# Optimization experiments

Measured on AMD Instinct MI355X. Metric: run time of the kernel, lower is better.

Reference implementation:

```python
import jax, jax.numpy as jnp
import numpy as np

N = 50000      # num_nodes
F_IN = 128     # num_features
E = 800000     # num edges (before self-loops)
H1, D1 = 8, 16 # conv1: 8 heads x 16 dims -> 128 concat
D2 = 8         # conv2: 1 head x 8 dims
NEG_SLOPE = 0.2


def setup_inputs() -> dict:
    key = jax.random.key(0)
    ks = jax.random.split(key, 16)
    s = 0.05
    return {
        "x": jax.random.normal(ks[0], (N, F_IN), jnp.float32),
        "edge_index": jax.random.randint(ks[1], (2, E), 0, N, dtype=jnp.int64),
        "W1": jax.random.normal(ks[2], (F_IN, H1 * D1), jnp.float32) * s,
        "att_src1": jax.random.normal(ks[3], (H1, D1), jnp.float32) * s,
        "att_dst1": jax.random.normal(ks[4], (H1, D1), jnp.float32) * s,
        "b1": jnp.zeros((H1 * D1,), jnp.float32),
        "W2": jax.random.normal(ks[5], (H1 * D1, D2), jnp.float32) * s,
        "att_src2": jax.random.normal(ks[6], (1, D2), jnp.float32) * s,
        "att_dst2": jax.random.normal(ks[7], (1, D2), jnp.float32) * s,
        "b2": jnp.zeros((D2,), jnp.float32),
        "fc1_w": jax.random.normal(ks[8], (N * D2, 84), jnp.float32) * 0.005,
        "fc1_b": jnp.zeros((84,), jnp.float32),
        "fc2_w": jax.random.normal(ks[9], (84, 24), jnp.float32) * s,
        "fc2_b": jnp.zeros((24,), jnp.float32),
        "fc3_w": jax.random.normal(ks[10], (24, 2), jnp.float32) * s,
        "fc3_b": jnp.zeros((2,), jnp.float32),
    }


def gat_conv(x, src, dst, W, att_src, att_dst, bias, heads, out_dim):
    """PyG GATConv: per-head linear, edge attention, scatter-softmax over
    incoming edges per target node, weighted scatter-add aggregation."""
    n = x.shape[0]
    h = (x @ W).reshape(n, heads, out_dim)            # [N,H,D]
    a_src = jnp.einsum('nhd,hd->nh', h, att_src)      # [N,H]
    a_dst = jnp.einsum('nhd,hd->nh', h, att_dst)      # [N,H]
    e = jax.nn.leaky_relu(a_src[src] + a_dst[dst], NEG_SLOPE)  # [Et,H]
    # softmax over edges grouped by destination node (stable)
    m = jax.ops.segment_max(e, dst, num_segments=n)
    p = jnp.exp(e - m[dst])
    denom = jax.ops.segment_sum(p, dst, num_segments=n)
    alpha = p / denom[dst]                            # [Et,H]
    out = jax.ops.segment_sum(alpha[:, :, None] * h[src], dst, num_segments=n)
    return out.reshape(n, heads * out_dim) + bias


def reference(x, edge_index, W1, att_src1, att_dst1, b1,
              W2, att_src2, att_dst2, b2,
              fc1_w, fc1_b, fc2_w, fc2_b, fc3_w, fc3_b):
    # add self-loops (GATConv default add_self_loops=True)
    loop = jnp.arange(N, dtype=edge_index.dtype)
    src = jnp.concatenate([edge_index[0], loop])
    dst = jnp.concatenate([edge_index[1], loop])

    h = jax.nn.elu(gat_conv(x, src, dst, W1, att_src1, att_dst1, b1, H1, D1))
    h = jax.nn.elu(gat_conv(h, src, dst, W2, att_src2, att_dst2, b2, 1, D2))

    z = h.reshape(1, N * D2)                          # batch of one graph
    z = jax.nn.elu(z @ fc1_w + fc1_b)
    z = jax.nn.elu(z @ fc2_w + fc2_b)
    z = z @ fc3_w + fc3_b
    return jax.nn.log_softmax(z, axis=1)              # [1,2]
```

## Files before the change

### kernel.cpp

```cpp
#include <hip/hip_runtime.h>
#include <math.h>

#define N_NODES 50000
#define F_IN 128
#define NE 800000
#define NH1 8
#define ND1 16
#define ND2 8
#define NEG 0.2f
#define ZLEN (N_NODES * ND2)
#define NBLK 196
#define FC1_RPB 240
#define FC1_NB 1667

typedef __attribute__((ext_vector_type(8))) short bf16x8;
typedef __attribute__((ext_vector_type(4))) float f32x4;

__device__ __forceinline__ float lrelu(float v) { return v > 0.f ? v : NEG * v; }
__device__ __forceinline__ float elu1(float v)  { return v > 0.f ? v : (__expf(v) - 1.f); }

__device__ __forceinline__ unsigned short f2bf(float f) {
    union { float f; unsigned int i; } c; c.f = f;
    unsigned int u = c.i;
    return (unsigned short)((u + 0x7FFFu + ((u >> 16) & 1u)) >> 16);
}
__device__ __forceinline__ float bflo(unsigned int u) {
    union { unsigned int i; float f; } c; c.i = u << 16; return c.f;
}
__device__ __forceinline__ float bfhi(unsigned int u) {
    union { unsigned int i; float f; } c; c.i = u & 0xFFFF0000u; return c.f;
}
__device__ __forceinline__ int ei_is64(const int* __restrict__ ei) {
    return ((ei[1] | ei[3] | ei[5] | ei[7]) == 0) ? 1 : 0;
}

__global__ __launch_bounds__(256) void prep_kernel(const float* __restrict__ W,
                                                   uint4* __restrict__ wbf,
                                                   int* __restrict__ counts) {
    int i = blockIdx.x * 256 + threadIdx.x;
    if (i < N_NODES) counts[i] = 1;
    if (i < 2048) {
        int col = i >> 4, kc = i & 15;
        unsigned int u[4];
        #pragma unroll
        for (int jj = 0; jj < 4; ++jj) {
            unsigned int lo = f2bf(W[(kc * 8 + 2 * jj) * 128 + col]);
            unsigned int hi = f2bf(W[(kc * 8 + 2 * jj + 1) * 128 + col]);
            u[jj] = lo | (hi << 16);
        }
        uint4 v; v.x = u[0]; v.y = u[1]; v.z = u[2]; v.w = u[3];
        wbf[col * 16 + (kc ^ (col & 15))] = v;
    }
}

__global__ void hist_kernel(const int* __restrict__ ei, int* __restrict__ counts) {
    int t = blockIdx.x * blockDim.x + threadIdx.x;
    if (t * 4 >= NE) return;
    int d0, d1, d2, d3;
    if (ei_is64(ei)) {
        const int4* p = reinterpret_cast<const int4*>(ei + 2 * NE);
        int4 a = p[t * 2];
        int4 b = p[t * 2 + 1];
        d0 = a.x; d1 = a.z; d2 = b.x; d3 = b.z;
    } else {
        int4 a = reinterpret_cast<const int4*>(ei + NE)[t];
        d0 = a.x; d1 = a.y; d2 = a.z; d3 = a.w;
    }
    atomicAdd(&counts[d0], 1);
    atomicAdd(&counts[d1], 1);
    atomicAdd(&counts[d2], 1);
    atomicAdd(&counts[d3], 1);
}

__global__ __launch_bounds__(256) void scan1_kernel(const int* __restrict__ counts,
                                                    int* __restrict__ bsum) {
    const int t = threadIdx.x;
    int i = blockIdx.x * 256 + t;
    int v = (i < N_NODES) ? counts[i] : 0;
    #pragma unroll
    for (int off = 32; off; off >>= 1) v += __shfl_down(v, off, 64);
    __shared__ int ws[4];
    if ((t & 63) == 0) ws[t >> 6] = v;
    __syncthreads();
    if (t == 0) bsum[blockIdx.x] = ws[0] + ws[1] + ws[2] + ws[3];
}

__global__ __launch_bounds__(256) void scan3_kernel(const int* __restrict__ counts,
                                                    const int* __restrict__ bsum,
                                                    int* __restrict__ rowptr,
                                                    int* __restrict__ cursor) {
    __shared__ int wsum[4];
    __shared__ int wpre[4];
    __shared__ int s_boff;
    const int t = threadIdx.x;
    const int lane = t & 63, w = t >> 6;
    int i = blockIdx.x * 256 + t;
    int v = (i < N_NODES) ? counts[i] : 0;
    int incl = v;
    #pragma unroll
    for (int off = 1; off < 64; off <<= 1) {
        int u = __shfl_up(incl, off, 64);
        if (lane >= off) incl += u;
    }
    if (lane == 63) wsum[w] = incl;
    if (t < 64) {
        int s = 0;
        for (int k = t; k < blockIdx.x; k += 64) s += bsum[k];
        #pragma unroll
        for (int off = 32; off; off >>= 1) s += __shfl_down(s, off, 64);
        if (t == 0) s_boff = s;
    }
    __syncthreads();
    if (t == 0) { int s = 0; for (int j = 0; j < 4; ++j) { wpre[j] = s; s += wsum[j]; } }
    __syncthreads();
    incl += wpre[w] + s_boff;
    if (i < N_NODES) { rowptr[i + 1] = incl; cursor[i] = incl - v; }
    if (i == 0) rowptr[0] = 0;
}

__global__ void fill_kernel(const int* __restrict__ ei,
                            int* __restrict__ cursor, int* __restrict__ esrc) {
    const int t = blockIdx.x * blockDim.x + threadIdx.x;
    const int NT_E = NE / 4;
    if (t < NT_E) {
        int s0, s1, s2, s3, d0, d1, d2, d3;
        if (ei_is64(ei)) {
            const int4* ps = reinterpret_cast<const int4*>(ei);
            const int4* pd = reinterpret_cast<const int4*>(ei + 2 * NE);
            int4 sa = ps[t * 2], sb = ps[t * 2 + 1];
            int4 da = pd[t * 2], db = pd[t * 2 + 1];
            s0 = sa.x; s1 = sa.z; s2 = sb.x; s3 = sb.z;
            d0 = da.x; d1 = da.z; d2 = db.x; d3 = db.z;
        } else {
            int4 sa = reinterpret_cast<const int4*>(ei)[t];
            int4 da = reinterpret_cast<const int4*>(ei + NE)[t];
            s0 = sa.x; s1 = sa.y; s2 = sa.z; s3 = sa.w;
            d0 = da.x; d1 = da.y; d2 = da.z; d3 = da.w;
        }
        esrc[atomicAdd(&cursor[d0], 1)] = s0;
        esrc[atomicAdd(&cursor[d1], 1)] = s1;
        esrc[atomicAdd(&cursor[d2], 1)] = s2;
        esrc[atomicAdd(&cursor[d3], 1)] = s3;
    } else {
        int i = t - NT_E;
        if (i < N_NODES) esrc[atomicAdd(&cursor[i], 1)] = i;
    }
}

__global__ __launch_bounds__(256) void gemm1_kernel(const float* __restrict__ x,
                                                    const uint4* __restrict__ wbf,
                                                    const float* __restrict__ att_src,
                                                    const float* __restrict__ att_dst,
                                                    unsigned int* __restrict__ h1b,
                                                    float* __restrict__ a_src1,
                                                    float* __restrict__ a_dst1) {
    __shared__ uint4 Xs[1024];
    __shared__ uint4 Ws[2048];
    const int t = threadIdx.x;
    const int row0 = blockIdx.x * 64;

    #pragma unroll
    for (int p = 0; p < 8; ++p) Ws[p * 256 + t] = wbf[p * 256 + t];

    #pragma unroll
    for (int p = 0; p < 4; ++p) {
        int cidx = p * 256 + t;
        int row = cidx >> 4, c = cidx & 15;
        int grow = row0 + row;
        float4 xa = make_float4(0.f, 0.f, 0.f, 0.f);
        float4 xb = make_float4(0.f, 0.f, 0.f, 0.f);
        if (grow < N_NODES) {
            xa = *reinterpret_cast<const float4*>(x + (size_t)grow * F_IN + c * 8);
            xb = *reinterpret_cast<const float4*>(x + (size_t)grow * F_IN + c * 8 + 4);
        }
        uint4 u;
        u.x = (unsigned int)f2bf(xa.x) | ((unsigned int)f2bf(xa.y) << 16);
        u.y = (unsigned int)f2bf(xa.z) | ((unsigned int)f2bf(xa.w) << 16);
        u.z = (unsigned int)f2bf(xb.x) | ((unsigned int)f2bf(xb.y) << 16);
        u.w = (unsigned int)f2bf(xb.z) | ((unsigned int)f2bf(xb.w) << 16);
        Xs[row * 16 + (c ^ (row & 15))] = u;
    }
    __syncthreads();

    const int wv = t >> 6;
    const int l  = t & 63;
    const int d  = l & 15;
    const int g  = l >> 4;
    const int arow = wv * 16 + d;

    f32x4 acc[8];
    #pragma unroll
    for (int n = 0; n < 8; ++n) { acc[n][0] = 0.f; acc[n][1] = 0.f; acc[n][2] = 0.f; acc[n][3] = 0.f; }

    #pragma unroll
    for (int ks = 0; ks < 4; ++ks) {
        int kc = ks * 4 + g;
        union { uint4 u; bf16x8 v; } A;
        A.u = Xs[arow * 16 + (kc ^ d)];
        #pragma unroll
        for (int n = 0; n < 8; ++n) {
            union { uint4 u; bf16x8 v; } B;
            B.u = Ws[(n * 16 + d) * 16 + (kc ^ d)];
            acc[n] = __builtin_amdgcn_mfma_f32_16x16x32_bf16(A.v, B.v, acc[n], 0, 0, 0);
        }
    }

    float as8[8], ad8[8];
    #pragma unroll
    for (int n = 0; n < 8; ++n) { as8[n] = att_src[n * 16 + d]; ad8[n] = att_dst[n * 16 + d]; }
    #pragma unroll
    for (int n = 0; n < 8; ++n) {
        #pragma unroll
        for (int r = 0; r < 4; ++r) {
            float ps = acc[n][r] * as8[n];
            float pd = acc[n][r] * ad8[n];
            #pragma unroll
            for (int off = 1; off < 16; off <<= 1) {
                ps += __shfl_xor(ps, off, 16);
                pd += __shfl_xor(pd, off, 16);
            }
            int grow = row0 + wv * 16 + g * 4 + r;
            if (d == 0 && grow < N_NODES) {
                a_src1[grow * 8 + n] = ps;
                a_dst1[grow * 8 + n] = pd;
            }
        }
    }
    #pragma unroll
    for (int n = 0; n < 8; ++n) {
        #pragma unroll
        for (int r = 0; r < 4; ++r) {
            float lo = acc[n][r];
            float hi = __shfl_xor(lo, 1, 64);
            int grow = row0 + wv * 16 + g * 4 + r;
            if (((d & 1) == 0) && grow < N_NODES) {
                unsigned int u = (unsigned int)f2bf(lo) | ((unsigned int)f2bf(hi) << 16);
                h1b[(size_t)grow * 64 + n * 8 + (d >> 1)] = u;
            }
        }
    }
}

__global__ __launch_bounds__(256) void agg1_kernel(const unsigned int* __restrict__ h1b,
                                                   const float* __restrict__ a_src,
                                                   const float* __restrict__ a_dst,
                                                   const int* __restrict__ rowptr,
                                                   const int* __restrict__ esrc,
                                                   const float* __restrict__ b1,
                                                   float* __restrict__ hout) {
    int wid = (blockIdx.x * 256 + threadIdx.x) >> 6;
    if (wid >= N_NODES) return;
    const int lane = threadIdx.x & 63;
    const int h = lane >> 3;
    const float ad = a_dst[wid * 8 + h];
    float acc0 = 0.f, acc1 = 0.f, den = 0.f;
    int j = rowptr[wid];
    const int jend = rowptr[wid + 1];
    for (; j + 8 <= jend; j += 8) {
        int s[8];
        #pragma unroll
        for (int k = 0; k < 8; ++k) s[k] = esrc[j + k];
        unsigned int u[8];
        #pragma unroll
        for (int k = 0; k < 8; ++k) u[k] = h1b[(size_t)s[k] * 64 + lane];
        float e[8];
        #pragma unroll
        for (int k = 0; k < 8; ++k) e[k] = a_src[s[k] * 8 + h];
        #pragma unroll
        for (int k = 0; k < 8; ++k) {
            float p = __expf(lrelu(e[k] + ad));
            den += p;
            acc0 = fmaf(p, bflo(u[k]), acc0);
            acc1 = fmaf(p, bfhi(u[k]), acc1);
        }
    }
    for (; j + 4 <= jend; j += 4) {
        int s0 = esrc[j], s1 = esrc[j + 1], s2 = esrc[j + 2], s3 = esrc[j + 3];
        unsigned int u0 = h1b[(size_t)s0 * 64 + lane];
        unsigned int u1 = h1b[(size_t)s1 * 64 + lane];
        unsigned int u2 = h1b[(size_t)s2 * 64 + lane];
        unsigned int u3 = h1b[(size_t)s3 * 64 + lane];
        float e0 = a_src[s0 * 8 + h], e1 = a_src[s1 * 8 + h];
        float e2 = a_src[s2 * 8 + h], e3 = a_src[s3 * 8 + h];
        float p0 = __expf(lrelu(e0 + ad));
        float p1 = __expf(lrelu(e1 + ad));
        float p2 = __expf(lrelu(e2 + ad));
        float p3 = __expf(lrelu(e3 + ad));
        den += (p0 + p1) + (p2 + p3);
        acc0 = fmaf(p0, bflo(u0), acc0); acc1 = fmaf(p0, bfhi(u0), acc1);
        acc0 = fmaf(p1, bflo(u1), acc0); acc1 = fmaf(p1, bfhi(u1), acc1);
        acc0 = fmaf(p2, bflo(u2), acc0); acc1 = fmaf(p2, bfhi(u2), acc1);
        acc0 = fmaf(p3, bflo(u3), acc0); acc1 = fmaf(p3, bfhi(u3), acc1);
    }
    for (; j < jend; ++j) {
        int s = esrc[j];
        unsigned int u = h1b[(size_t)s * 64 + lane];
        float e = a_src[s * 8 + h];
        float p = __expf(lrelu(e + ad));
        den += p;
        acc0 = fmaf(p, bflo(u), acc0);
        acc1 = fmaf(p, bfhi(u), acc1);
    }
    float inv = 1.f / den;
    float2 bb = *reinterpret_cast<const float2*>(b1 + 2 * lane);
    float o0 = elu1(acc0 * inv + bb.x);
    float o1 = elu1(acc1 * inv + bb.y);
    *reinterpret_cast<float2*>(hout + (size_t)wid * F_IN + 2 * lane) = make_float2(o0, o1);
}

__global__ __launch_bounds__(256) void gemm2_kernel(const float* __restrict__ h,
                                                    const float* __restrict__ W2,
                                                    const float* __restrict__ att_src2,
                                                    const float* __restrict__ att_dst2,
                                                    float* __restrict__ h2,
                                                    float* __restrict__ a_src2,
                                                    float* __restrict__ a_dst2) {
    __shared__ float Ws[F_IN * ND2];
    __shared__ float Hs[32 * 132];
    int t = threadIdx.x;
    int node0 = blockIdx.x * 32;
    #pragma unroll
    for (int i = 0; i < 4; ++i) { int idx = i * 256 + t; Ws[idx] = W2[idx]; }
    #pragma unroll
    for (int i = 0; i < 4; ++i) {
        int fidx = i * 256 + t;
        int r = fidx >> 5;
        int c4 = fidx & 31;
        int grow = node0 + r;
        float4 v = make_float4(0.f, 0.f, 0.f, 0.f);
        if (grow < N_NODES) v = *reinterpret_cast<const float4*>(h + (size_t)grow * F_IN + c4 * 4);
        *reinterpret_cast<float4*>(&Hs[r * 132 + c4 * 4]) = v;
    }
    __syncthreads();
    int nsub = t >> 3, d = t & 7;
    int node = node0 + nsub;
    float acc = 0.f;
    #pragma unroll 8
    for (int k = 0; k < F_IN; ++k)
        acc = fmaf(Hs[nsub * 132 + k], Ws[k * ND2 + d], acc);
    float vs = acc * att_src2[d];
    float vd = acc * att_dst2[d];
    #pragma unroll
    for (int off = 4; off >= 1; off >>= 1) {
        vs += __shfl_xor(vs, off, 8);
        vd += __shfl_xor(vd, off, 8);
    }
    if (node < N_NODES) {
        h2[node * ND2 + d] = acc;
        if (d == 0) { a_src2[node] = vs; a_dst2[node] = vd; }
    }
}

__global__ void agg2_kernel(const float* __restrict__ h2,
                            const float* __restrict__ a_src2, const float* __restrict__ a_dst2,
                            const int* __restrict__ rowptr, const int* __restrict__ esrc,
                            const float* __restrict__ b2, float* __restrict__ g) {
    int n = blockIdx.x * blockDim.x + threadIdx.x;
    if (n >= N_NODES) return;
    float ad = a_dst2[n];
    float acc[8] = {0.f, 0.f, 0.f, 0.f, 0.f, 0.f, 0.f, 0.f};
    float den = 0.f;
    int jend = rowptr[n + 1];
    for (int j = rowptr[n]; j < jend; ++j) {
        int s = esrc[j];
        float p = __expf(lrelu(a_src2[s] + ad));
        den += p;
        float4 va = *reinterpret_cast<const float4*>(h2 + s * ND2);
        float4 vb = *reinterpret_cast<const float4*>(h2 + s * ND2 + 4);
        acc[0] = fmaf(p, va.x, acc[0]); acc[1] = fmaf(p, va.y, acc[1]);
        acc[2] = fmaf(p, va.z, acc[2]); acc[3] = fmaf(p, va.w, acc[3]);
        acc[4] = fmaf(p, vb.x, acc[4]); acc[5] = fmaf(p, vb.y, acc[5]);
        acc[6] = fmaf(p, vb.z, acc[6]); acc[7] = fmaf(p, vb.w, acc[7]);
    }
    float inv = 1.f / den;
    float4 o0 = make_float4(elu1(acc[0] * inv + b2[0]), elu1(acc[1] * inv + b2[1]),
                            elu1(acc[2] * inv + b2[2]), elu1(acc[3] * inv + b2[3]));
    float4 o1 = make_float4(elu1(acc[4] * inv + b2[4]), elu1(acc[5] * inv + b2[5]),
                            elu1(acc[6] * inv + b2[6]), elu1(acc[7] * inv + b2[7]));
    *reinterpret_cast<float4*>(g + n * ND2)     = o0;
    *reinterpret_cast<float4*>(g + n * ND2 + 4) = o1;
}

__global__ __launch_bounds__(256) void fc1_stage1(const float* __restrict__ z,
                                                  const float* __restrict__ w,
                                                  float* __restrict__ partial) {
    __shared__ float zs[FC1_RPB];
    __shared__ float4 red[252];
    const int t = threadIdx.x;
    const int b = blockIdx.x;
    const int r0 = b * FC1_RPB;
    if (t < FC1_RPB) {
        int gr = r0 + t;
        zs[t] = (gr < ZLEN) ? z[gr] : 0.f;
    }
    __syncthreads();
    const int c4 = t % 21;
    const int rr = t / 21;
    if (t < 252) {
        float4 a = make_float4(0.f, 0.f, 0.f, 0.f);
        const float4* __restrict__ w4 = reinterpret_cast<const float4*>(w);
        if (r0 + FC1_RPB <= ZLEN) {
            #pragma unroll
            for (int bq = 0; bq < 5; ++bq) {
                float4 wv[4];
                float  zv[4];
                #pragma unroll
                for (int u = 0; u < 4; ++u) {
                    int i = bq * 48 + u * 12 + rr;
                    wv[u] = w4[(size_t)(r0 + i) * 21 + c4];
                    zv[u] = zs[i];
                }
                #pragma unroll
                for (int u = 0; u < 4; ++u) {
                    a.x = fmaf(zv[u], wv[u].x, a.x);
                    a.y = fmaf(zv[u], wv[u].y, a.y);
                    a.z = fmaf(zv[u], wv[u].z, a.z);
                    a.w = fmaf(zv[u], wv[u].w, a.w);
                }
            }
        } else {
            for (int i = rr; i < FC1_RPB; i += 12) {
                if (r0 + i < ZLEN) {
                    float4 wv = w4[(size_t)(r0 + i) * 21 + c4];
                    float  zv = zs[i];
                    a.x = fmaf(zv, wv.x, a.x); a.y = fmaf(zv, wv.y, a.y);
                    a.z = fmaf(zv, wv.z, a.z); a.w = fmaf(zv, wv.w, a.w);
                }
            }
        }
        red[t] = a;
    }
    __syncthreads();
    if (t < 21) {
        float4 s = red[t];
        #pragma unroll
        for (int k = 1; k < 12; ++k) {
            float4 v = red[k * 21 + t];
            s.x += v.x; s.y += v.y; s.z += v.z; s.w += v.w;
        }
        *reinterpret_cast<float4*>(partial + (size_t)b * 88 + t * 4) = s;
    }
}

__global__ __launch_bounds__(1024) void fctail_kernel(const float* __restrict__ partial,
                                                      const float* __restrict__ fc1_b,
                                                      const float* __restrict__ fc2_w,
                                                      const float* __restrict__ fc2_b,
                                                      const float* __restrict__ fc3_w,
                                                      const float* __restrict__ fc3_b,
                                                      float* __restrict__ out) {
    __shared__ float red[1008];
    __shared__ float z1[84];
    __shared__ float z2[24];
    const int t = threadIdx.x;
    if (t < 1008) {
        const int j  = t % 84;
        const int sl = t / 84;
        float s = 0.f;
        for (int b = sl; b < FC1_NB; b += 12)
            s += partial[(size_t)b * 88 + j];
        red[t] = s;
    }
    __syncthreads();
    if (t < 84) {
        float s = 0.f;
        #pragma unroll
        for (int sl = 0; sl < 12; ++sl) s += red[sl * 84 + t];
        z1[t] = elu1(s + fc1_b[t]);
    }
    __syncthreads();
    if (t < 24) {
        float a = fc2_b[t];
        for (int i = 0; i < 84; ++i) a = fmaf(z1[i], fc2_w[i * 24 + t], a);
        z2[t] = elu1(a);
    }
    __syncthreads();
    if (t == 0) {
        float z3[2];
        #pragma unroll
        for (int jj = 0; jj < 2; ++jj) {
            float a = fc3_b[jj];
            for (int i = 0; i < 24; ++i) a = fmaf(z2[i], fc3_w[i * 2 + jj], a);
            z3[jj] = a;
        }
        float m = fmaxf(z3[0], z3[1]);
        float l = m + logf(__expf(z3[0] - m) + __expf(z3[1] - m));
        out[0] = z3[0] - l;
        out[1] = z3[1] - l;
    }
}

extern "C" void kernel_launch(void* const* d_in, const int* in_sizes, int n_in,
                              void* d_out, int out_size, void* d_ws, size_t ws_size,
                              hipStream_t stream) {
    const float* x        = (const float*)d_in[0];
    const int*   ei       = (const int*)d_in[1];
    const float* W1       = (const float*)d_in[2];
    const float* att_src1 = (const float*)d_in[3];
    const float* att_dst1 = (const float*)d_in[4];
    const float* b1       = (const float*)d_in[5];
    const float* W2       = (const float*)d_in[6];
    const float* att_src2 = (const float*)d_in[7];
    const float* att_dst2 = (const float*)d_in[8];
    const float* b2       = (const float*)d_in[9];
    const float* fc1_w    = (const float*)d_in[10];
    const float* fc1_b    = (const float*)d_in[11];
    const float* fc2_w    = (const float*)d_in[12];
    const float* fc2_b    = (const float*)d_in[13];
    const float* fc3_w    = (const float*)d_in[14];
    const float* fc3_b    = (const float*)d_in[15];
    float* out = (float*)d_out;

    char* ws = (char*)d_ws;
    unsigned int* h1b = (unsigned int*)(ws + 0);
    float* hbuf   = (float*)(ws + 12800000);
    float* a_src1 = (float*)(ws + 38400000);
    float* a_dst1 = (float*)(ws + 40000000);
    float* h2     = (float*)(ws + 41600000);
    float* a_src2 = (float*)(ws + 43200000);
    float* a_dst2 = (float*)(ws + 43400000);
    float* g      = (float*)(ws + 43600000);
    int*   counts = (int*)  (ws + 45200000);
    int*   rowptr = (int*)  (ws + 45400000);
    int*   cursor = (int*)  (ws + 45600064);
    int*   esrc   = (int*)  (ws + 45800064);
    float* partial= (float*)(ws + 49200064);
    uint4* wbf    = (uint4*)(ws + 49786848);
    int*   bsum   = (int*)  (ws + 49819616);

    prep_kernel<<<NBLK, 256, 0, stream>>>(W1, wbf, counts);
    hist_kernel<<<(NE / 4 + 255) / 256, 256, 0, stream>>>(ei, counts);
    scan1_kernel<<<NBLK, 256, 0, stream>>>(counts, bsum);
    scan3_kernel<<<NBLK, 256, 0, stream>>>(counts, bsum, rowptr, cursor);
    fill_kernel<<<(NE / 4 + N_NODES + 255) / 256, 256, 0, stream>>>(ei, cursor, esrc);

    gemm1_kernel<<<(N_NODES + 63) / 64, 256, 0, stream>>>(x, wbf, att_src1, att_dst1, h1b, a_src1, a_dst1);
    agg1_kernel<<<(N_NODES + 3) / 4, 256, 0, stream>>>(h1b, a_src1, a_dst1, rowptr, esrc, b1, hbuf);

    gemm2_kernel<<<(N_NODES + 31) / 32, 256, 0, stream>>>(hbuf, W2, att_src2, att_dst2, h2, a_src2, a_dst2);
    agg2_kernel<<<(N_NODES + 255) / 256, 256, 0, stream>>>(h2, a_src2, a_dst2, rowptr, esrc, b2, g);

    fc1_stage1<<<FC1_NB, 256, 0, stream>>>(g, fc1_w, partial);
    fctail_kernel<<<1, 1024, 0, stream>>>(partial, fc1_b, fc2_w, fc2_b, fc3_w, fc3_b, out);
}
```

Measured before the change: 250.3 us.

## Store layer-1 features in FP8 and split edges across half-wavefronts in aggregation

The layer-1 projected features are now packed as FP8 (4 values per 32-bit word) instead of bf16, halving the per-row gather footprint from 256 to 128 bytes. The aggregation kernel splits each node's edge list between the two 32-lane halves of the wavefront, each lane handling 4 features, and combines partial sums with a cross-half shuffle. This targets the memory-bound random gather in agg1, at the cost of lower feature precision (FP8 e4m3) that may affect accuracy tolerance.

```diff
diff --git a/kernel.cpp b/kernel.cpp
--- a/kernel.cpp
+++ b/kernel.cpp
@@ -15,6 +15,7 @@
 
 typedef __attribute__((ext_vector_type(8))) short bf16x8;
 typedef __attribute__((ext_vector_type(4))) float f32x4;
+typedef __attribute__((ext_vector_type(2))) float f32x2;
 
 __device__ __forceinline__ float lrelu(float v) { return v > 0.f ? v : NEG * v; }
 __device__ __forceinline__ float elu1(float v)  { return v > 0.f ? v : (__expf(v) - 1.f); }
@@ -23,12 +24,6 @@
     union { float f; unsigned int i; } c; c.f = f;
     unsigned int u = c.i;
     return (unsigned short)((u + 0x7FFFu + ((u >> 16) & 1u)) >> 16);
-}
-__device__ __forceinline__ float bflo(unsigned int u) {
-    union { unsigned int i; float f; } c; c.i = u << 16; return c.f;
-}
-__device__ __forceinline__ float bfhi(unsigned int u) {
-    union { unsigned int i; float f; } c; c.i = u & 0xFFFF0000u; return c.f;
 }
 __device__ __forceinline__ int ei_is64(const int* __restrict__ ei) {
     return ((ei[1] | ei[3] | ei[5] | ei[7]) == 0) ? 1 : 0;
@@ -151,7 +146,7 @@
                                                     const uint4* __restrict__ wbf,
                                                     const float* __restrict__ att_src,
                                                     const float* __restrict__ att_dst,
-                                                    unsigned int* __restrict__ h1b,
+                                                    unsigned int* __restrict__ h1f8,
                                                     float* __restrict__ a_src1,
                                                     float* __restrict__ a_dst1) {
     __shared__ uint4 Xs[1024];
@@ -230,18 +225,20 @@
     for (int n = 0; n < 8; ++n) {
         #pragma unroll
         for (int r = 0; r < 4; ++r) {
-            float lo = acc[n][r];
-            float hi = __shfl_xor(lo, 1, 64);
+            float v = acc[n][r];
+            float v1 = __shfl_xor(v, 1, 64);
+            int p01 = __builtin_amdgcn_cvt_pk_fp8_f32(v, v1, 0, false);
+            int p23 = __shfl_xor(p01, 2, 64);
             int grow = row0 + wv * 16 + g * 4 + r;
-            if (((d & 1) == 0) && grow < N_NODES) {
-                unsigned int u = (unsigned int)f2bf(lo) | ((unsigned int)f2bf(hi) << 16);
-                h1b[(size_t)grow * 64 + n * 8 + (d >> 1)] = u;
+            if (((d & 3) == 0) && grow < N_NODES) {
+                unsigned int u = ((unsigned int)p01 & 0xFFFFu) | ((unsigned int)p23 << 16);
+                h1f8[(size_t)grow * 32 + n * 4 + (d >> 2)] = u;
             }
         }
     }
 }
 
-__global__ __launch_bounds__(256) void agg1_kernel(const unsigned int* __restrict__ h1b,
+__global__ __launch_bounds__(256) void agg1_kernel(const unsigned int* __restrict__ h1f8,
                                                    const float* __restrict__ a_src,
                                                    const float* __restrict__ a_dst,
                                                    const int* __restrict__ rowptr,
@@ -251,61 +248,59 @@
     int wid = (blockIdx.x * 256 + threadIdx.x) >> 6;
     if (wid >= N_NODES) return;
     const int lane = threadIdx.x & 63;
-    const int h = lane >> 3;
+    const int m    = lane & 31;
+    const int half = lane >> 5;
+    const int h    = m >> 2;
     const float ad = a_dst[wid * 8 + h];
-    float acc0 = 0.f, acc1 = 0.f, den = 0.f;
+    float a0 = 0.f, a1 = 0.f, a2 = 0.f, a3 = 0.f, den = 0.f;
     int j = rowptr[wid];
     const int jend = rowptr[wid + 1];
     for (; j + 8 <= jend; j += 8) {
-        int s[8];
-        #pragma unroll
-        for (int k = 0; k < 8; ++k) s[k] = esrc[j + k];
-        unsigned int u[8];
-        #pragma unroll
-        for (int k = 0; k < 8; ++k) u[k] = h1b[(size_t)s[k] * 64 + lane];
-        float e[8];
-        #pragma unroll
-        for (int k = 0; k < 8; ++k) e[k] = a_src[s[k] * 8 + h];
-        #pragma unroll
-        for (int k = 0; k < 8; ++k) {
+        int s[4];
+        #pragma unroll
+        for (int k = 0; k < 4; ++k) s[k] = esrc[j + 2 * k + half];
+        unsigned int u[4];
+        #pragma unroll
+        for (int k = 0; k < 4; ++k) u[k] = h1f8[(size_t)s[k] * 32 + m];
+        float e[4];
+        #pragma unroll
+        for (int k = 0; k < 4; ++k) e[k] = a_src[s[k] * 8 + h];
+        #pragma unroll
+        for (int k = 0; k < 4; ++k) {
             float p = __expf(lrelu(e[k] + ad));
             den += p;
-            acc0 = fmaf(p, bflo(u[k]), acc0);
-            acc1 = fmaf(p, bfhi(u[k]), acc1);
-        }
-    }
-    for (; j + 4 <= jend; j += 4) {
-        int s0 = esrc[j], s1 = esrc[j + 1], s2 = esrc[j + 2], s3 = esrc[j + 3];
-        unsigned int u0 = h1b[(size_t)s0 * 64 + lane];
-        unsigned int u1 = h1b[(size_t)s1 * 64 + lane];
-        unsigned int u2 = h1b[(size_t)s2 * 64 + lane];
-        unsigned int u3 = h1b[(size_t)s3 * 64 + lane];
-        float e0 = a_src[s0 * 8 + h], e1 = a_src[s1 * 8 + h];
-        float e2 = a_src[s2 * 8 + h], e3 = a_src[s3 * 8 + h];
-        float p0 = __expf(lrelu(e0 + ad));
-        float p1 = __expf(lrelu(e1 + ad));
-        float p2 = __expf(lrelu(e2 + ad));
-        float p3 = __expf(lrelu(e3 + ad));
-        den += (p0 + p1) + (p2 + p3);
-        acc0 = fmaf(p0, bflo(u0), acc0); acc1 = fmaf(p0, bfhi(u0), acc1);
-        acc0 = fmaf(p1, bflo(u1), acc0); acc1 = fmaf(p1, bfhi(u1), acc1);
-        acc0 = fmaf(p2, bflo(u2), acc0); acc1 = fmaf(p2, bfhi(u2), acc1);
-        acc0 = fmaf(p3, bflo(u3), acc0); acc1 = fmaf(p3, bfhi(u3), acc1);
-    }
-    for (; j < jend; ++j) {
-        int s = esrc[j];
-        unsigned int u = h1b[(size_t)s * 64 + lane];
-        float e = a_src[s * 8 + h];
-        float p = __expf(lrelu(e + ad));
-        den += p;
-        acc0 = fmaf(p, bflo(u), acc0);
-        acc1 = fmaf(p, bfhi(u), acc1);
-    }
-    float inv = 1.f / den;
-    float2 bb = *reinterpret_cast<const float2*>(b1 + 2 * lane);
-    float o0 = elu1(acc0 * inv + bb.x);
-    float o1 = elu1(acc1 * inv + bb.y);
-    *reinterpret_cast<float2*>(hout + (size_t)wid * F_IN + 2 * lane) = make_float2(o0, o1);
+            f32x2 lo = __builtin_amdgcn_cvt_pk_f32_fp8(u[k], false);
+            f32x2 hi = __builtin_amdgcn_cvt_pk_f32_fp8(u[k], true);
+            a0 = fmaf(p, lo[0], a0); a1 = fmaf(p, lo[1], a1);
+            a2 = fmaf(p, hi[0], a2); a3 = fmaf(p, hi[1], a3);
+        }
+    }
+    for (; j < jend; j += 2) {
+        int e_idx = j + half;
+        if (e_idx < jend) {
+            int s = esrc[e_idx];
+            unsigned int u = h1f8[(size_t)s * 32 + m];
+            float e = a_src[s * 8 + h];
+            float p = __expf(lrelu(e + ad));
+            den += p;
+            f32x2 lo = __builtin_amdgcn_cvt_pk_f32_fp8(u, false);
+            f32x2 hi = __builtin_amdgcn_cvt_pk_f32_fp8(u, true);
+            a0 = fmaf(p, lo[0], a0); a1 = fmaf(p, lo[1], a1);
+            a2 = fmaf(p, hi[0], a2); a3 = fmaf(p, hi[1], a3);
+        }
+    }
+    a0  += __shfl_xor(a0, 32, 64);
+    a1  += __shfl_xor(a1, 32, 64);
+    a2  += __shfl_xor(a2, 32, 64);
+    a3  += __shfl_xor(a3, 32, 64);
+    den += __shfl_xor(den, 32, 64);
+    if (half == 0) {
+        float inv = 1.f / den;
+        float4 bb = *reinterpret_cast<const float4*>(b1 + 4 * m);
+        float4 o = make_float4(elu1(a0 * inv + bb.x), elu1(a1 * inv + bb.y),
+                               elu1(a2 * inv + bb.z), elu1(a3 * inv + bb.w));
+        *reinterpret_cast<float4*>(hout + (size_t)wid * F_IN + 4 * m) = o;
+    }
 }
 
 __global__ __launch_bounds__(256) void gemm2_kernel(const float* __restrict__ h,
@@ -512,21 +507,21 @@
     float* out = (float*)d_out;
 
     char* ws = (char*)d_ws;
-    unsigned int* h1b = (unsigned int*)(ws + 0);
-    float* hbuf   = (float*)(ws + 12800000);
-    float* a_src1 = (float*)(ws + 38400000);
-    float* a_dst1 = (float*)(ws + 40000000);
-    float* h2     = (float*)(ws + 41600000);
-    float* a_src2 = (float*)(ws + 43200000);
-    float* a_dst2 = (float*)(ws + 43400000);
-    float* g      = (float*)(ws + 43600000);
-    int*   counts = (int*)  (ws + 45200000);
-    int*   rowptr = (int*)  (ws + 45400000);
-    int*   cursor = (int*)  (ws + 45600064);
-    int*   esrc   = (int*)  (ws + 45800064);
-    float* partial= (float*)(ws + 49200064);
-    uint4* wbf    = (uint4*)(ws + 49786848);
-    int*   bsum   = (int*)  (ws + 49819616);
+    unsigned int* h1f8 = (unsigned int*)(ws + 0);
+    float* hbuf   = (float*)(ws + 6400000);
+    float* a_src1 = (float*)(ws + 32000000);
+    float* a_dst1 = (float*)(ws + 33600000);
+    float* h2     = (float*)(ws + 35200000);
+    float* a_src2 = (float*)(ws + 36800000);
+    float* a_dst2 = (float*)(ws + 37000000);
+    float* g      = (float*)(ws + 37200000);
+    int*   counts = (int*)  (ws + 38800000);
+    int*   rowptr = (int*)  (ws + 39000000);
+    int*   cursor = (int*)  (ws + 39200064);
+    int*   esrc   = (int*)  (ws + 39400064);
+    float* partial= (float*)(ws + 42800064);
+    uint4* wbf    = (uint4*)(ws + 43386848);
+    int*   bsum   = (int*)  (ws + 43419616);
 
     prep_kernel<<<NBLK, 256, 0, stream>>>(W1, wbf, counts);
     hist_kernel<<<(NE / 4 + 255) / 256, 256, 0, stream>>>(ei, counts);
@@ -534,8 +529,8 @@
     scan3_kernel<<<NBLK, 256, 0, stream>>>(counts, bsum, rowptr, cursor);
     fill_kernel<<<(NE / 4 + N_NODES + 255) / 256, 256, 0, stream>>>(ei, cursor, esrc);
 
-    gemm1_kernel<<<(N_NODES + 63) / 64, 256, 0, stream>>>(x, wbf, att_src1, att_dst1, h1b, a_src1, a_dst1);
-    agg1_kernel<<<(N_NODES + 3) / 4, 256, 0, stream>>>(h1b, a_src1, a_dst1, rowptr, esrc, b1, hbuf);
+    gemm1_kernel<<<(N_NODES + 63) / 64, 256, 0, stream>>>(x, wbf, att_src1, att_dst1, h1f8, a_src1, a_dst1);
+    agg1_kernel<<<(N_NODES + 3) / 4, 256, 0, stream>>>(h1f8, a_src1, a_dst1, rowptr, esrc, b1, hbuf);
 
     gemm2_kernel<<<(N_NODES + 31) / 32, 256, 0, stream>>>(hbuf, W2, att_src2, att_dst2, h2, a_src2, a_dst2);
     agg2_kernel<<<(N_NODES + 255) / 256, 256, 0, stream>>>(h2, a_src2, a_dst2, rowptr, esrc, b2, g);
```

New measurement: 243.2 us. -2.9%, faster.
